# Kernel tuning notes

Measured on AMD Instinct MI355X. Metric: run time of the kernel, lower is better.

Reference implementation:

```python
import jax, jax.numpy as jnp
import numpy as np

INS, OUTS = 768, 64
B, S = 8, 2048


def setup_inputs() -> dict:
    key = jax.random.key(0)
    ks = jax.random.split(key, 7)
    scale = 1.0 / np.sqrt(INS)
    inputs = jax.random.normal(ks[0], (B, S, INS), dtype=jnp.float32)
    Wq = jax.random.uniform(ks[1], (INS, OUTS), jnp.float32, -scale, scale)
    bq = jax.random.uniform(ks[2], (OUTS,), jnp.float32, -scale, scale)
    Wk = jax.random.uniform(ks[3], (INS, OUTS), jnp.float32, -scale, scale)
    bk = jax.random.uniform(ks[4], (OUTS,), jnp.float32, -scale, scale)
    Wv = jax.random.uniform(ks[5], (INS, OUTS), jnp.float32, -scale, scale)
    bv = jax.random.uniform(ks[6], (OUTS,), jnp.float32, -scale, scale)
    return {"inputs": inputs, "Wq": Wq, "bq": bq, "Wk": Wk, "bk": bk, "Wv": Wv, "bv": bv}


def reference(inputs, Wq, bq, Wk, bk, Wv, bv):
    # QKV projections: [B, S, ins] @ [ins, outs] -> [B, S, outs]
    q = jnp.einsum('bsi,io->bso', inputs, Wq) + bq
    k = jnp.einsum('bsi,io->bso', inputs, Wk) + bk
    v = jnp.einsum('bsi,io->bso', inputs, Wv) + bv
    dim_k = k.shape[-1]
    # scores: [B, S, S] (materialized, as in the original bmm-based impl)
    att = jnp.einsum('bqd,bkd->bqk', q, k) / jnp.sqrt(jnp.asarray(dim_k, q.dtype))
    att_soft = jax.nn.softmax(att, axis=-1)
    out = jnp.einsum('bqk,bkd->bqd', att_soft, v)
    return out
```

## Files before the change

### kernel.cpp

```cpp
#include <hip/hip_runtime.h>
#include <hip/hip_bf16.h>
#include <stdint.h>

#define INS 768
#define OUTS 64
#define BB 8
#define SS 2048
#define LDP 40

typedef __attribute__((ext_vector_type(8))) short short8;
typedef __attribute__((ext_vector_type(4))) float f32x4;

__device__ inline unsigned short f2bf(float f) {
  union { float f; uint32_t u; } v; v.f = f;
  uint32_t r = v.u + 0x7FFFu + ((v.u >> 16) & 1u);
  return (unsigned short)(r >> 16);
}

__device__ inline short8 cvt8hw(float4 a, float4 b) {
  union { __hip_bfloat162 h[4]; short8 s; } u;
  u.h[0] = __float22bfloat162_rn(make_float2(a.x, a.y));
  u.h[1] = __float22bfloat162_rn(make_float2(a.z, a.w));
  u.h[2] = __float22bfloat162_rn(make_float2(b.x, b.y));
  u.h[3] = __float22bfloat162_rn(make_float2(b.z, b.w));
  return u.s;
}

__device__ inline void gl_lds16(const void* g, void* l) {
  __builtin_amdgcn_global_load_lds(
      (const __attribute__((address_space(1))) uint32_t*)g,
      (__attribute__((address_space(3))) uint32_t*)l, 16, 0, 0);
}

__global__ __launch_bounds__(256) void prep(
    const float* __restrict__ Wq, const float* __restrict__ Wk,
    const float* __restrict__ Wv, unsigned short* __restrict__ WT) {
  const int idx = blockIdx.x * 256 + threadIdx.x;
  const int m = idx / (INS * OUTS);
  const int r = idx - m * (INS * OUTS);
  const int k = r >> 6, n = r & 63;
  const float* W = (m == 0) ? Wq : (m == 1) ? Wk : Wv;
  const float s = (m == 0) ? 0.125f : 1.0f;
  WT[((size_t)m * OUTS + n) * INS + k] = f2bf(W[(size_t)k * OUTS + n] * s);
}

__global__ __launch_bounds__(256) void qkv(
    const float* __restrict__ X, const unsigned short* __restrict__ WT,
    const float* __restrict__ bq, const float* __restrict__ bk,
    const float* __restrict__ bv,
    unsigned short* __restrict__ Qg, unsigned short* __restrict__ Kg,
    unsigned short* __restrict__ Vtg) {
  __shared__ __align__(16) float Xs[2][1024];
  const int tid  = threadIdx.x;
  const int wave = tid >> 6, lane = tid & 63;
  const int quad = lane >> 4, l16 = lane & 15;
  const int chg  = wave;
  const int row0 = blockIdx.x * 32;

  const int sr = tid >> 3, ss = tid & 7;
  const char* gsrc =
      (const char*)(X + (size_t)(row0 + sr) * INS) + ((ss ^ (sr & 7)) << 4);
  char* ldst = (char*)&Xs[0][0] + wave * 1024;

  const float* Bm[3]; float scl[3]; int col0[3];
  const unsigned short* Wt[3];
#pragma unroll
  for (int nt = 0; nt < 3; ++nt) {
    const int n0 = chg * 48 + nt * 16;
    const int mat = n0 >> 6;
    col0[nt] = n0 & 63;
    Wt[nt] = WT + ((size_t)mat * OUTS + col0[nt] + l16) * INS + quad * 8;
    if (mat == 0)      { Bm[nt] = bq; scl[nt] = 0.125f; }
    else if (mat == 1) { Bm[nt] = bk; scl[nt] = 1.0f; }
    else               { Bm[nt] = bv; scl[nt] = 1.0f; }
  }

  int off0[2], off1[2];
#pragma unroll
  for (int fr = 0; fr < 2; ++fr) {
    const int lr = fr * 16 + l16;
    off0[fr] = lr * 128 + ((((quad << 1)    ) ^ (lr & 7)) << 4);
    off1[fr] = lr * 128 + ((((quad << 1) | 1) ^ (lr & 7)) << 4);
  }

  f32x4 acc[2][3];
#pragma unroll
  for (int fr = 0; fr < 2; ++fr)
#pragma unroll
    for (int nt = 0; nt < 3; ++nt) acc[fr][nt] = (f32x4){0.f, 0.f, 0.f, 0.f};

  short8 wb[2][3];

  gl_lds16(gsrc, ldst);
#pragma unroll
  for (int nt = 0; nt < 3; ++nt)
    wb[0][nt] = *reinterpret_cast<const short8*>(Wt[nt]);
  __syncthreads();

#pragma unroll
  for (int kc = 0; kc < 24; ++kc) {
    const int cur = kc & 1;
    if (kc + 1 < 24) {
      gl_lds16(gsrc + (size_t)(kc + 1) * 128, ldst + ((cur ^ 1) << 12));
#pragma unroll
      for (int nt = 0; nt < 3; ++nt)
        wb[(kc + 1) & 1][nt] =
            *reinterpret_cast<const short8*>(Wt[nt] + (kc + 1) * 32);
    }
    const char* xb = (const char*)&Xs[cur][0];
    float4 f00 = *reinterpret_cast<const float4*>(xb + off0[0]);
    float4 f01 = *reinterpret_cast<const float4*>(xb + off1[0]);
    float4 f10 = *reinterpret_cast<const float4*>(xb + off0[1]);
    float4 f11 = *reinterpret_cast<const float4*>(xb + off1[1]);
    short8 a0 = cvt8hw(f00, f01);
    short8 a1 = cvt8hw(f10, f11);
#pragma unroll
    for (int nt = 0; nt < 3; ++nt) {
      acc[0][nt] = __builtin_amdgcn_mfma_f32_16x16x32_bf16(a0, wb[cur][nt], acc[0][nt], 0, 0, 0);
      acc[1][nt] = __builtin_amdgcn_mfma_f32_16x16x32_bf16(a1, wb[cur][nt], acc[1][nt], 0, 0, 0);
    }
    __syncthreads();
  }

#pragma unroll
  for (int fr = 0; fr < 2; ++fr) {
    const int gm0 = row0 + fr * 16 + quad * 4;
#pragma unroll
    for (int nt = 0; nt < 3; ++nt) {
      const int n = chg * 48 + nt * 16 + l16;
      const float bias = Bm[nt][col0[nt] + l16] * scl[nt];
      if (n < 128) {
        unsigned short* dstbase = (n < 64) ? Qg : Kg;
        const int nn = n & 63;
#pragma unroll
        for (int r = 0; r < 4; ++r)
          dstbase[(size_t)(gm0 + r) * OUTS + nn] = f2bf(acc[fr][nt][r] + bias);
      } else {
        const int d = n - 128;
        const int batch = gm0 >> 11, s0 = gm0 & 2047;
        ushort4 pk;
        pk.x = f2bf(acc[fr][nt][0] + bias);
        pk.y = f2bf(acc[fr][nt][1] + bias);
        pk.z = f2bf(acc[fr][nt][2] + bias);
        pk.w = f2bf(acc[fr][nt][3] + bias);
        *reinterpret_cast<ushort4*>(&Vtg[((size_t)batch * OUTS + d) * SS + s0]) = pk;
      }
    }
  }
}

__global__ __launch_bounds__(256) void attn(
    const unsigned short* __restrict__ Qg, const unsigned short* __restrict__ Kg,
    const unsigned short* __restrict__ Vtg,
    float* __restrict__ OP, float* __restrict__ LS) {
  __shared__ __align__(16) unsigned short Ps[4][2][16 * LDP];
  const int tid  = threadIdx.x;
  const int wave = tid >> 6, lane = tid & 63;
  const int quad = lane >> 4, l16 = lane & 15;
  const int bt  = blockIdx.x >> 6;
  const int rem = blockIdx.x & 63;
  const int qb  = rem >> 2, ksl = rem & 3;
  const int q0 = qb * 128 + wave * 32;
  const unsigned short* Qb = Qg + (size_t)bt * SS * OUTS;
  const unsigned short* Kb = Kg + (size_t)bt * SS * OUTS;
  const unsigned short* Vb = Vtg + (size_t)bt * OUTS * SS;

  short8 aq[2][2];
#pragma unroll
  for (int mh = 0; mh < 2; ++mh)
#pragma unroll
    for (int ks = 0; ks < 2; ++ks)
      aq[mh][ks] = *reinterpret_cast<const short8*>(
          Qb + (size_t)(q0 + mh * 16 + l16) * OUTS + ks * 32 + quad * 8);

  f32x4 oacc[2][4];
#pragma unroll
  for (int mh = 0; mh < 2; ++mh)
#pragma unroll
    for (int nt = 0; nt < 4; ++nt) oacc[mh][nt] = (f32x4){0.f, 0.f, 0.f, 0.f};
  float lsum[2][4] = {{0.f,0.f,0.f,0.f},{0.f,0.f,0.f,0.f}};

  const int jbeg = ksl * 512;
  for (int j0 = jbeg; j0 < jbeg + 512; j0 += 32) {
    short8 bk[2][2], bv[4];
#pragma unroll
    for (int nt2 = 0; nt2 < 2; ++nt2)
#pragma unroll
      for (int ks = 0; ks < 2; ++ks)
        bk[nt2][ks] = *reinterpret_cast<const short8*>(
            Kb + (size_t)(j0 + nt2 * 16 + l16) * OUTS + ks * 32 + quad * 8);
#pragma unroll
    for (int nt = 0; nt < 4; ++nt)
      bv[nt] = *reinterpret_cast<const short8*>(
          Vb + (size_t)(nt * 16 + l16) * SS + j0 + quad * 8);

#pragma unroll
    for (int mh = 0; mh < 2; ++mh) {
      f32x4 sc[2];
      sc[0] = (f32x4){0.f,0.f,0.f,0.f}; sc[1] = (f32x4){0.f,0.f,0.f,0.f};
#pragma unroll
      for (int ks = 0; ks < 2; ++ks)
#pragma unroll
        for (int nt2 = 0; nt2 < 2; ++nt2)
          sc[nt2] = __builtin_amdgcn_mfma_f32_16x16x32_bf16(aq[mh][ks], bk[nt2][ks], sc[nt2], 0, 0, 0);

      unsigned short* Pw = Ps[wave][mh];
#pragma unroll
      for (int nt2 = 0; nt2 < 2; ++nt2)
#pragma unroll
        for (int r = 0; r < 4; ++r) {
          float p = __expf(sc[nt2][r]);
          lsum[mh][r] += p;
          Pw[(quad * 4 + r) * LDP + nt2 * 16 + l16] = f2bf(p);
        }
      short8 ap = *reinterpret_cast<const short8*>(&Pw[l16 * LDP + quad * 8]);
#pragma unroll
      for (int nt = 0; nt < 4; ++nt)
        oacc[mh][nt] = __builtin_amdgcn_mfma_f32_16x16x32_bf16(ap, bv[nt], oacc[mh][nt], 0, 0, 0);
    }
  }

#pragma unroll
  for (int st = 1; st < 16; st <<= 1)
#pragma unroll
    for (int mh = 0; mh < 2; ++mh)
#pragma unroll
      for (int r = 0; r < 4; ++r) lsum[mh][r] += __shfl_xor(lsum[mh][r], st, 64);

  float* OPb = OP + ((size_t)ksl * BB + bt) * SS * OUTS;
#pragma unroll
  for (int mh = 0; mh < 2; ++mh)
#pragma unroll
    for (int nt = 0; nt < 4; ++nt)
#pragma unroll
      for (int r = 0; r < 4; ++r) {
        int q = q0 + mh * 16 + quad * 4 + r;
        OPb[(size_t)q * OUTS + nt * 16 + l16] = oacc[mh][nt][r];
      }
  if (l16 == 0) {
#pragma unroll
    for (int mh = 0; mh < 2; ++mh)
#pragma unroll
      for (int r = 0; r < 4; ++r)
        LS[(size_t)ksl * BB * SS + bt * SS + q0 + mh * 16 + quad * 4 + r] = lsum[mh][r];
  }
}

__global__ __launch_bounds__(256) void combine(
    const float* __restrict__ OP, const float* __restrict__ LS,
    float* __restrict__ out) {
  const size_t i4 = (size_t)blockIdx.x * 256 + threadIdx.x;
  const size_t row = (i4 * 4) >> 6;
  float4 o = make_float4(0.f, 0.f, 0.f, 0.f);
  float l = 0.f;
#pragma unroll
  for (int ks = 0; ks < 4; ++ks) {
    float4 t = reinterpret_cast<const float4*>(OP + (size_t)ks * BB * SS * OUTS)[i4];
    o.x += t.x; o.y += t.y; o.z += t.z; o.w += t.w;
    l += LS[(size_t)ks * BB * SS + row];
  }
  const float inv = 1.0f / l;
  reinterpret_cast<float4*>(out)[i4] = make_float4(o.x * inv, o.y * inv, o.z * inv, o.w * inv);
}

extern "C" void kernel_launch(void* const* d_in, const int* in_sizes, int n_in,
                              void* d_out, int out_size, void* d_ws, size_t ws_size,
                              hipStream_t stream) {
  const float* X  = (const float*)d_in[0];
  const float* Wq = (const float*)d_in[1];
  const float* bq = (const float*)d_in[2];
  const float* Wk = (const float*)d_in[3];
  const float* bk = (const float*)d_in[4];
  const float* Wv = (const float*)d_in[5];
  const float* bv = (const float*)d_in[6];
  float* out = (float*)d_out;

  char* ws = (char*)d_ws;
  unsigned short* Qg  = (unsigned short*)(ws);
  unsigned short* Kg  = (unsigned short*)(ws + (size_t)2 * 1024 * 1024);
  unsigned short* Vtg = (unsigned short*)(ws + (size_t)4 * 1024 * 1024);
  unsigned short* WT  = (unsigned short*)(ws + (size_t)6 * 1024 * 1024);
  float*          OP  = (float*)(ws + (size_t)7 * 1024 * 1024);
  float*          LS  = (float*)(ws + (size_t)23 * 1024 * 1024);

  prep<<<576, 256, 0, stream>>>(Wq, Wk, Wv, WT);
  qkv<<<512, 256, 0, stream>>>(X, WT, bq, bk, bv, Qg, Kg, Vtg);
  attn<<<512, 256, 0, stream>>>(Qg, Kg, Vtg, OP, LS);
  combine<<<1024, 256, 0, stream>>>(OP, LS, out);
}
```

Before: 155.0 us.

## Stage K/V tiles through double-buffered LDS with async global-to-LDS loads

Instead of each wave loading its K and V^T fragments straight from global memory, the attention kernel now cooperatively loads 32-key K and V tiles into double-buffered LDS using direct global-to-LDS copies, with XOR swizzling to avoid bank conflicts. The next tile is prefetched while the current one is consumed, and a block barrier ends each iteration. This removes redundant global loads across the four waves and overlaps memory with MFMA work, at the cost of a per-iteration __syncthreads and extra LDS use.

```diff
diff --git a/kernel.cpp b/kernel.cpp
--- a/kernel.cpp
+++ b/kernel.cpp
@@ -153,6 +153,8 @@
     const unsigned short* __restrict__ Qg, const unsigned short* __restrict__ Kg,
     const unsigned short* __restrict__ Vtg,
     float* __restrict__ OP, float* __restrict__ LS) {
+  __shared__ __align__(16) char KsB[2][4096];
+  __shared__ __align__(16) char VsB[2][4096];
   __shared__ __align__(16) unsigned short Ps[4][2][16 * LDP];
   const int tid  = threadIdx.x;
   const int wave = tid >> 6, lane = tid & 63;
@@ -164,6 +166,15 @@
   const unsigned short* Qb = Qg + (size_t)bt * SS * OUTS;
   const unsigned short* Kb = Kg + (size_t)bt * SS * OUTS;
   const unsigned short* Vb = Vtg + (size_t)bt * OUTS * SS;
+  const int jbeg = ksl * 512;
+
+  const int krow = wave * 8 + (lane >> 3), ks8 = lane & 7;
+  const int vrow = wave * 16 + (lane >> 2), vs4 = lane & 3;
+  const int vsw  = (vrow & 3) ^ ((vrow >> 2) & 3);
+  const char* ksrc = (const char*)(Kb + (size_t)(jbeg + krow) * OUTS) +
+                     ((ks8 ^ (krow & 7)) << 4);
+  const char* vsrc = (const char*)(Vb + (size_t)vrow * SS + jbeg) +
+                     ((vs4 ^ vsw) << 4);
 
   short8 aq[2][2];
 #pragma unroll
@@ -173,6 +184,20 @@
       aq[mh][ks] = *reinterpret_cast<const short8*>(
           Qb + (size_t)(q0 + mh * 16 + l16) * OUTS + ks * 32 + quad * 8);
 
+  int koff[2][2];
+#pragma unroll
+  for (int nt2 = 0; nt2 < 2; ++nt2)
+#pragma unroll
+    for (int ks = 0; ks < 2; ++ks)
+      koff[nt2][ks] = (nt2 * 16 + l16) * 128 +
+                      ((((ks << 2) | quad) ^ (l16 & 7)) << 4);
+  int voff[4];
+#pragma unroll
+  for (int nt = 0; nt < 4; ++nt) {
+    const int dr = nt * 16 + l16;
+    voff[nt] = dr * 64 + ((quad ^ ((dr & 3) ^ ((dr >> 2) & 3))) << 4);
+  }
+
   f32x4 oacc[2][4];
 #pragma unroll
   for (int mh = 0; mh < 2; ++mh)
@@ -180,19 +205,27 @@
     for (int nt = 0; nt < 4; ++nt) oacc[mh][nt] = (f32x4){0.f, 0.f, 0.f, 0.f};
   float lsum[2][4] = {{0.f,0.f,0.f,0.f},{0.f,0.f,0.f,0.f}};
 
-  const int jbeg = ksl * 512;
-  for (int j0 = jbeg; j0 < jbeg + 512; j0 += 32) {
+  gl_lds16(ksrc, &KsB[0][0] + wave * 1024);
+  gl_lds16(vsrc, &VsB[0][0] + wave * 1024);
+  __syncthreads();
+
+  for (int kc = 0; kc < 16; ++kc) {
+    const int cur = kc & 1;
+    if (kc + 1 < 16) {
+      gl_lds16(ksrc + (size_t)(kc + 1) * 4096, &KsB[cur ^ 1][0] + wave * 1024);
+      gl_lds16(vsrc + (size_t)(kc + 1) * 64,   &VsB[cur ^ 1][0] + wave * 1024);
+    }
+    const char* kb8 = &KsB[cur][0];
+    const char* vb8 = &VsB[cur][0];
     short8 bk[2][2], bv[4];
 #pragma unroll
     for (int nt2 = 0; nt2 < 2; ++nt2)
 #pragma unroll
       for (int ks = 0; ks < 2; ++ks)
-        bk[nt2][ks] = *reinterpret_cast<const short8*>(
-            Kb + (size_t)(j0 + nt2 * 16 + l16) * OUTS + ks * 32 + quad * 8);
+        bk[nt2][ks] = *reinterpret_cast<const short8*>(kb8 + koff[nt2][ks]);
 #pragma unroll
     for (int nt = 0; nt < 4; ++nt)
-      bv[nt] = *reinterpret_cast<const short8*>(
-          Vb + (size_t)(nt * 16 + l16) * SS + j0 + quad * 8);
+      bv[nt] = *reinterpret_cast<const short8*>(vb8 + voff[nt]);
 
 #pragma unroll
     for (int mh = 0; mh < 2; ++mh) {
@@ -218,6 +251,7 @@
       for (int nt = 0; nt < 4; ++nt)
         oacc[mh][nt] = __builtin_amdgcn_mfma_f32_16x16x32_bf16(ap, bv[nt], oacc[mh][nt], 0, 0, 0);
     }
+    __syncthreads();
   }
 
 #pragma unroll
```

Measured after the change: 144.1 us. 7.0% less time.
